# Performance work log

Hardware: AMD Instinct MI355X
Metric: run time of the kernel (lower is better)

The kernel has to match this reference:

```python
import jax, jax.numpy as jnp
import numpy as np

B, C_IN, C_INT, C_OUT, H, W = 4, 1024, 256, 1024, 64, 64
EPS = 1e-5

def conv1x1(x, w, b):
    # x: (B, Cin, H, W), w: (Cout, Cin), b: (Cout,)
    return jnp.einsum('bchw,oc->bohw', x, w) + b[None, :, None, None]

def batchnorm_eval(x, gamma, beta, mean, var):
    inv = gamma / jnp.sqrt(var + EPS)
    return x * inv[None, :, None, None] + (beta - mean * inv)[None, :, None, None]

def setup_inputs() -> dict:
    key = jax.random.key(0)
    ks = jax.random.split(key, 8)
    s_in = 1.0 / np.sqrt(C_IN)
    s_int = 1.0 / np.sqrt(C_INT)
    return {
        'x': jax.random.normal(ks[0], (B, C_IN, H, W), dtype=jnp.float32),
        'w_key': jax.random.normal(ks[1], (C_INT, C_IN), dtype=jnp.float32) * s_in,
        'b_key': jnp.zeros((C_INT,), dtype=jnp.float32),
        'gamma': jnp.ones((C_INT,), dtype=jnp.float32),
        'beta': jnp.zeros((C_INT,), dtype=jnp.float32),
        'mean': jnp.zeros((C_INT,), dtype=jnp.float32),
        'var': jnp.ones((C_INT,), dtype=jnp.float32),
        'w_value': jax.random.normal(ks[2], (C_INT, C_IN), dtype=jnp.float32) * s_in,
        'b_value': jax.random.normal(ks[3], (C_INT,), dtype=jnp.float32) * 0.1,
        'w_out': jax.random.normal(ks[4], (C_OUT, C_INT), dtype=jnp.float32) * s_int,
        'b_out': jax.random.normal(ks[5], (C_OUT,), dtype=jnp.float32) * 0.1,
    }

def reference(x, w_key, b_key, gamma, beta, mean, var, w_value, b_value, w_out, b_out):
    Bb, _, h, w = x.shape
    N = h * w
    # value: 1x1 conv, (B, C, N) -> (B, N, C)
    value = conv1x1(x, w_value, b_value).reshape(Bb, C_INT, N).transpose(0, 2, 1)
    # query/key share the same conv+BN (f_query = f_key)
    qk = batchnorm_eval(conv1x1(x, w_key, b_key), gamma, beta, mean, var).reshape(Bb, C_INT, N)
    query = qk.transpose(0, 2, 1)  # (B, N, C)
    key = qk                        # (B, C, N)
    sim = jnp.einsum('bnc,bcm->bnm', query, key) * (C_INT ** -0.5)  # (B, N, N)
    sim = jax.nn.softmax(sim, axis=-1)
    context = jnp.einsum('bnm,bmc->bnc', sim, value)  # (B, N, C)
    context = context.transpose(0, 2, 1).reshape(Bb, C_INT, h, w)
    return conv1x1(context, w_out, b_out)
```

## Files before the change

### kernel.cpp

```cpp
#include <hip/hip_runtime.h>

#define BATCH 4
#define CIN   1024
#define CI    256
#define CO    1024
#define NSP   4096

typedef __attribute__((ext_vector_type(8))) short bf16x8;
typedef __attribute__((ext_vector_type(4))) float f32x4;
typedef __attribute__((ext_vector_type(2))) unsigned uint2v;

struct __align__(8) us4 { unsigned short x, y, z, w; };

#define DEVI __device__ __forceinline__

DEVI unsigned short f2bf(float f) {
  union { float f; unsigned u; } un; un.f = f;
  unsigned u = un.u;
  u += 0x7FFFu + ((u >> 16) & 1u);
  return (unsigned short)(u >> 16);
}

DEVI unsigned cvtpk(float lo, float hi) {
  unsigned r;
  asm("v_cvt_pk_bf16_f32 %0, %1, %2" : "=v"(r) : "v"(lo), "v"(hi));
  return r;
}

DEVI void gl2lds16(const void* g, void* l) {
  __builtin_amdgcn_global_load_lds(
      (const __attribute__((address_space(1))) void*)g,
      (__attribute__((address_space(3))) void*)l, 16, 0, 0);
}

DEVI f32x4 mfma16(bf16x8 a, bf16x8 b, f32x4 c) {
  return __builtin_amdgcn_mfma_f32_16x16x32_bf16(a, b, c, 0, 0, 0);
}

__global__ __launch_bounds__(256) void k_xpose_prep(
    const float* __restrict__ x, unsigned short* __restrict__ xT,
    const float* __restrict__ w_key, const float* __restrict__ w_val,
    const float* __restrict__ w_out,
    const float* __restrict__ gamma, const float* __restrict__ beta,
    const float* __restrict__ mean,  const float* __restrict__ var,
    const float* __restrict__ b_key,
    unsigned short* __restrict__ wkv, unsigned short* __restrict__ wob,
    float* __restrict__ sq, float* __restrict__ bq)
{
  int bid = blockIdx.x;
  if (bid < 2048) {
    int idx = bid * 256 + threadIdx.x;
    float wv = (idx < 262144) ? w_key[idx] : w_val[idx - 262144];
    wkv[idx] = f2bf(wv);
    if (idx < 262144) wob[idx] = f2bf(w_out[idx]);
    if (idx < 256) {
      float inv = gamma[idx] * rsqrtf(var[idx] + 1e-5f);
      sq[idx] = 0.25f * inv;
      bq[idx] = 0.25f * (beta[idx] + (b_key[idx] - mean[idx]) * inv);
    }
    return;
  }
  __shared__ unsigned short tile[64][66];
  int id2 = bid - 2048;
  int b = id2 >> 10, k0 = ((id2 >> 6) & 15) * 64, n0 = (id2 & 63) * 64;
  int tid = threadIdx.x;
  int rr = tid >> 4, cc = tid & 15;
  const float* xb = x + ((size_t)b * CIN + k0) * NSP + n0;
#pragma unroll
  for (int p = 0; p < 4; ++p) {
    int row = p * 16 + rr;
    float4 v = *(const float4*)(xb + (size_t)row * NSP + cc * 4);
    *(unsigned*)&tile[row][cc * 4 + 0] = cvtpk(v.x, v.y);
    *(unsigned*)&tile[row][cc * 4 + 2] = cvtpk(v.z, v.w);
  }
  __syncthreads();
  unsigned short* xtb = xT + ((size_t)b * NSP + n0) * CIN + k0;
#pragma unroll
  for (int p = 0; p < 4; ++p) {
    int n = p * 16 + rr;
    int kq = cc * 4;
    us4 pk;
    pk.x = tile[kq + 0][n]; pk.y = tile[kq + 1][n];
    pk.z = tile[kq + 2][n]; pk.w = tile[kq + 3][n];
    *(us4*)(xtb + (size_t)n * CIN + kq) = pk;
  }
}

template<int KDIM>
DEVI void gemm_core_db(const unsigned short* __restrict__ Ab,
                       const unsigned short* __restrict__ Bb,
                       unsigned short* ldsA, unsigned short* ldsB,
                       f32x4 acc[4][4], int tid)
{
  const int lane = tid & 63, wave = tid >> 6;
  const int q = lane >> 4, ln = lane & 15;
  const int wm = wave & 1, wn = wave >> 1;

  int aoff[4][2], boff[4][2];
#pragma unroll
  for (int f = 0; f < 4; ++f) {
    int ra = wm * 64 + f * 16 + ln;
    aoff[f][0] = (ra * 8 + ((q)     ^ (ra & 7))) * 8;
    aoff[f][1] = (ra * 8 + ((q + 4) ^ (ra & 7))) * 8;
    int rb = wn * 64 + f * 16 + ln;
    boff[f][0] = (rb * 8 + ((q)     ^ (rb & 7))) * 8;
    boff[f][1] = (rb * 8 + ((q + 4) ^ (rb & 7))) * 8;
  }
  int sgo[4];
#pragma unroll
  for (int i = 0; i < 4; ++i) {
    int s = i * 256 + tid;
    int row = s >> 3;
    int c8 = (s & 7) ^ (row & 7);
    sgo[i] = row * KDIM + c8 * 8;
  }
#pragma unroll
  for (int i = 0; i < 4; ++i) {
    gl2lds16(Ab + sgo[i], ldsA + (i * 256 + wave * 64) * 8);
    gl2lds16(Bb + sgo[i], ldsB + (i * 256 + wave * 64) * 8);
  }
  __syncthreads();

  for (int k0 = 0; k0 < KDIM; k0 += 64) {
    const int cur = (k0 >> 6) & 1;
    unsigned short* A = ldsA + cur * (128 * 64);
    unsigned short* B = ldsB + cur * (128 * 64);
    if (k0 + 64 < KDIM) {
      unsigned short* An = ldsA + (cur ^ 1) * (128 * 64);
      unsigned short* Bn = ldsB + (cur ^ 1) * (128 * 64);
#pragma unroll
      for (int i = 0; i < 4; ++i) {
        gl2lds16(Ab + sgo[i] + k0 + 64, An + (i * 256 + wave * 64) * 8);
        gl2lds16(Bb + sgo[i] + k0 + 64, Bn + (i * 256 + wave * 64) * 8);
      }
    }
#pragma unroll
    for (int kk = 0; kk < 2; ++kk) {
      bf16x8 af[4], bfr[4];
#pragma unroll
      for (int f = 0; f < 4; ++f) af[f]  = *(const bf16x8*)(A + aoff[f][kk]);
#pragma unroll
      for (int f = 0; f < 4; ++f) bfr[f] = *(const bf16x8*)(B + boff[f][kk]);
#pragma unroll
      for (int mf = 0; mf < 4; ++mf)
#pragma unroll
        for (int nf = 0; nf < 4; ++nf)
          acc[mf][nf] = mfma16(af[mf], bfr[nf], acc[mf][nf]);
    }
    __syncthreads();
  }
}

DEVI void gemm256(const unsigned short* __restrict__ Ab,
                  const unsigned short* __restrict__ Bb,
                  unsigned short* ldsA,
                  unsigned short* ldsB,
                  f32x4 acc[8][4], int tid)
{
  const int lane = tid & 63, wave = tid >> 6;
  const int q = lane >> 4, ln = lane & 15;
  const int wm = wave & 1, wn = wave >> 1;

  int aoff[8][2], boff[4][2];
#pragma unroll
  for (int f = 0; f < 8; ++f) {
    int ra = wm * 128 + f * 16 + ln;
    aoff[f][0] = (ra * 8 + ((q)     ^ (ra & 7))) * 8;
    aoff[f][1] = (ra * 8 + ((q + 4) ^ (ra & 7))) * 8;
  }
#pragma unroll
  for (int f = 0; f < 4; ++f) {
    int rb = wn * 64 + f * 16 + ln;
    boff[f][0] = (rb * 8 + ((q)     ^ (rb & 7))) * 8;
    boff[f][1] = (rb * 8 + ((q + 4) ^ (rb & 7))) * 8;
  }
  int sgoA[8], sgoB[4];
#pragma unroll
  for (int i = 0; i < 8; ++i) {
    int s = i * 256 + tid;
    int row = s >> 3;
    int c8 = (s & 7) ^ (row & 7);
    sgoA[i] = row * CI + c8 * 8;
  }
#pragma unroll
  for (int i = 0; i < 4; ++i) {
    int s = i * 256 + tid;
    int row = s >> 3;
    int c8 = (s & 7) ^ (row & 7);
    sgoB[i] = row * CI + c8 * 8;
  }
  for (int k0 = 0; k0 < CI; k0 += 64) {
#pragma unroll
    for (int i = 0; i < 8; ++i)
      gl2lds16(Ab + sgoA[i] + k0, ldsA + (i * 256 + wave * 64) * 8);
#pragma unroll
    for (int i = 0; i < 4; ++i)
      gl2lds16(Bb + sgoB[i] + k0, ldsB + (i * 256 + wave * 64) * 8);
    __syncthreads();
#pragma unroll
    for (int kk = 0; kk < 2; ++kk) {
      bf16x8 af[8], bfr[4];
#pragma unroll
      for (int f = 0; f < 8; ++f) af[f]  = *(const bf16x8*)(ldsA + aoff[f][kk]);
#pragma unroll
      for (int f = 0; f < 4; ++f) bfr[f] = *(const bf16x8*)(ldsB + boff[f][kk]);
#pragma unroll
      for (int mf = 0; mf < 8; ++mf)
#pragma unroll
        for (int nf = 0; nf < 4; ++nf)
          acc[mf][nf] = mfma16(af[mf], bfr[nf], acc[mf][nf]);
    }
    __syncthreads();
  }
}

__global__ __launch_bounds__(256) void k_convqkv(
    const unsigned short* __restrict__ wkv,
    const unsigned short* __restrict__ xT,
    const float* __restrict__ sq, const float* __restrict__ bq,
    const float* __restrict__ bval,
    unsigned short* __restrict__ qkT,
    unsigned short* __restrict__ vv)
{
  __shared__ __align__(16) unsigned short ldsA[2 * 128 * 64];
  __shared__ __align__(16) unsigned short ldsB[2 * 128 * 64];
  int b = blockIdx.z, m0 = blockIdx.y * 128, n0 = blockIdx.x * 128;
  int tid = threadIdx.x;
  f32x4 z = {0.f, 0.f, 0.f, 0.f};
  f32x4 acc[4][4];
#pragma unroll
  for (int i = 0; i < 4; ++i)
#pragma unroll
    for (int j = 0; j < 4; ++j) acc[i][j] = z;

  const unsigned short* wp = wkv + (size_t)m0 * CIN;
  const unsigned short* xp = xT + ((size_t)b * NSP + n0) * CIN;
  bool qk = (m0 < 256);
  gemm_core_db<CIN>(qk ? wp : xp, qk ? xp : wp, ldsA, ldsB, acc, tid);

  int lane = tid & 63, wave = tid >> 6, q = lane >> 4, ln = lane & 15;
  int wm = wave & 1, wn = wave >> 1;
  if (qk) {
#pragma unroll
    for (int mf = 0; mf < 4; ++mf) {
      int cb = m0 + wm * 64 + mf * 16 + q * 4;
      float s0_ = sq[cb + 0], s1_ = sq[cb + 1], s2_ = sq[cb + 2], s3_ = sq[cb + 3];
      float b0_ = bq[cb + 0], b1_ = bq[cb + 1], b2_ = bq[cb + 2], b3_ = bq[cb + 3];
#pragma unroll
      for (int nf = 0; nf < 4; ++nf) {
        int n = n0 + wn * 64 + nf * 16 + ln;
        uint2v pk2;
        pk2.x = cvtpk(acc[mf][nf][0] * s0_ + b0_, acc[mf][nf][1] * s1_ + b1_);
        pk2.y = cvtpk(acc[mf][nf][2] * s2_ + b2_, acc[mf][nf][3] * s3_ + b3_);
        *(uint2v*)(qkT + ((size_t)b * NSP + n) * CI + cb) = pk2;
      }
    }
  } else {
    int c0 = m0 - 256;
#pragma unroll
    for (int nf = 0; nf < 4; ++nf) {
      int c = c0 + wn * 64 + nf * 16 + ln;
      float bv = bval[c];
      unsigned short* vr = vv + ((size_t)b * CI + c) * NSP + n0 + wm * 64 + q * 4;
#pragma unroll
      for (int mf = 0; mf < 4; ++mf) {
        uint2v wv2;
        wv2.x = cvtpk(acc[mf][nf][0] + bv, acc[mf][nf][1] + bv);
        wv2.y = cvtpk(acc[mf][nf][2] + bv, acc[mf][nf][3] + bv);
        *(uint2v*)(vr + mf * 16) = wv2;
      }
    }
  }
}

__global__ __launch_bounds__(256, 2) void k_attn_part(
    const unsigned short* __restrict__ qkT,
    const unsigned short* __restrict__ vv,
    unsigned* __restrict__ Opart,
    float* __restrict__ Lpart)
{
  __shared__ __align__(16) unsigned short Kt[2][32 * 256];
  __shared__ __align__(16) unsigned short Vt[2][256 * 32];
  __shared__ __align__(16) unsigned short Pl[4 * 32 * 40];

  int bid = blockIdx.x;
  int slice = bid & 15, qt = bid >> 4;
  int b = slice >> 2, js = slice & 3;
  int n0 = qt * 128;
  int tid = threadIdx.x, lane = tid & 63, wave = tid >> 6;
  int q = lane >> 4, ln = lane & 15;
  const unsigned short* qkb = qkT + (size_t)b * NSP * CI;
  const unsigned short* vb  = vv  + (size_t)b * CI * NSP;

  bf16x8 Qf0[8], Qf1[8];
  {
    const unsigned short* qr0 = qkb + (size_t)(n0 + wave * 32 + ln) * CI + q * 8;
    const unsigned short* qr1 = qr0 + 16 * CI;
#pragma unroll
    for (int t = 0; t < 8; ++t) Qf0[t] = *(const bf16x8*)(qr0 + t * 32);
#pragma unroll
    for (int t = 0; t < 8; ++t) Qf1[t] = *(const bf16x8*)(qr1 + t * 32);
  }

  int kbA = (ln * 32 + ((q ^ (ln & 7)) & 7)) * 8;
  int kbB = (ln * 32 + (((4 + q) ^ (ln & 7)) & 7)) * 8;
  int vbase = (ln * 4 + ((q ^ ((ln >> 1) & 3)) & 3)) * 8;

  unsigned short* Plw = Pl + wave * (32 * 40);
  int pw0 = ln * 40 + q * 4;
  int pw1 = ln * 40 + 16 + q * 4;
  int pw2 = (ln + 16) * 40 + q * 4;
  int pw3 = (ln + 16) * 40 + 16 + q * 4;
  int pr0 = ln * 40 + q * 8;
  int pr1 = (ln + 16) * 40 + q * 8;

  int gko[4], gvo[4];
#pragma unroll
  for (int i = 0; i < 4; ++i) {
    int s = i * 256 + tid;
    int j = s >> 5, f = s & 31;
    gko[i] = j * CI + ((f & 24) | ((f ^ j) & 7)) * 8;
    int c = s >> 2;
    gvo[i] = c * NSP + ((s ^ (c >> 1)) & 3) * 8;
  }

  f32x4 O0[16], O1[16];
  f32x4 z = {0.f, 0.f, 0.f, 0.f};
#pragma unroll
  for (int cf = 0; cf < 16; ++cf) { O0[cf] = z; O1[cf] = z; }
  float l0c = 0.f, l1c = 0.f;

  int jbase = js * 1024;

#pragma unroll
  for (int i = 0; i < 4; ++i)
    gl2lds16(qkb + (size_t)jbase * CI + gko[i], &Kt[0][(i * 256 + wave * 64) * 8]);
#pragma unroll
  for (int i = 0; i < 4; ++i)
    gl2lds16(vb + jbase + gvo[i], &Vt[0][(i * 256 + wave * 64) * 8]);
  __syncthreads();

  for (int it = 0; it < 32; ++it) {
    int cur = it & 1;

    if (it < 31) {
      int j1 = jbase + (it + 1) * 32;
#pragma unroll
      for (int i = 0; i < 4; ++i)
        gl2lds16(qkb + (size_t)j1 * CI + gko[i],
                 &Kt[cur ^ 1][(i * 256 + wave * 64) * 8]);
#pragma unroll
      for (int i = 0; i < 4; ++i)
        gl2lds16(vb + j1 + gvo[i],
                 &Vt[cur ^ 1][(i * 256 + wave * 64) * 8]);
    }

    const unsigned short* Kc = Kt[cur];
    const unsigned short* Vc = Vt[cur];

    f32x4 s0 = z, s1 = z, s2 = z, s3 = z;
    __builtin_amdgcn_s_setprio(1);
#pragma unroll
    for (int t = 0; t < 8; ++t) {
      int ko = ((t & 1) ? kbB : kbA) + (t >> 1) * 64;
      bf16x8 kf0 = *(const bf16x8*)(Kc + ko);
      bf16x8 kf1 = *(const bf16x8*)(Kc + ko + 4096);
      s0 = mfma16(kf0, Qf0[t], s0);
      s1 = mfma16(kf1, Qf0[t], s1);
      s2 = mfma16(kf0, Qf1[t], s2);
      s3 = mfma16(kf1, Qf1[t], s3);
    }
    __builtin_amdgcn_s_setprio(0);

    float p00 = __expf(s0[0]), p01 = __expf(s0[1]);
    float p02 = __expf(s0[2]), p03 = __expf(s0[3]);
    float p04 = __expf(s1[0]), p05 = __expf(s1[1]);
    float p06 = __expf(s1[2]), p07 = __expf(s1[3]);
    float p10 = __expf(s2[0]), p11 = __expf(s2[1]);
    float p12 = __expf(s2[2]), p13 = __expf(s2[3]);
    float p14 = __expf(s3[0]), p15 = __expf(s3[1]);
    float p16 = __expf(s3[2]), p17 = __expf(s3[3]);

    uint2v w;
    w.x = cvtpk(p00, p01); w.y = cvtpk(p02, p03);
    *(uint2v*)(Plw + pw0) = w;
    w.x = cvtpk(p04, p05); w.y = cvtpk(p06, p07);
    *(uint2v*)(Plw + pw1) = w;
    w.x = cvtpk(p10, p11); w.y = cvtpk(p12, p13);
    *(uint2v*)(Plw + pw2) = w;
    w.x = cvtpk(p14, p15); w.y = cvtpk(p16, p17);
    *(uint2v*)(Plw + pw3) = w;

    l0c += ((p00 + p01) + (p02 + p03)) + ((p04 + p05) + (p06 + p07));
    l1c += ((p10 + p11) + (p12 + p13)) + ((p14 + p15) + (p16 + p17));

    bf16x8 pf0 = *(const bf16x8*)(Plw + pr0);
    bf16x8 pf1 = *(const bf16x8*)(Plw + pr1);
    __builtin_amdgcn_s_setprio(1);
#pragma unroll
    for (int cf = 0; cf < 16; ++cf) {
      bf16x8 vf = *(const bf16x8*)(Vc + vbase + cf * 512);
      O0[cf] = mfma16(pf0, vf, O0[cf]);
      O1[cf] = mfma16(pf1, vf, O1[cf]);
    }
    __builtin_amdgcn_s_setprio(0);

    __syncthreads();
  }

  l0c += __shfl_xor(l0c, 16); l0c += __shfl_xor(l0c, 32);
  l1c += __shfl_xor(l1c, 16); l1c += __shfl_xor(l1c, 32);

  unsigned* Ob = Opart + (size_t)bid * (64 * 256);
  if (lane < 16) {
    Lpart[bid * 128 + wave * 32 + lane] = l0c;
    Lpart[bid * 128 + wave * 32 + 16 + lane] = l1c;
  }
#pragma unroll
  for (int r = 0; r < 4; ++r) {
    int rp = wave * 16 + q * 4 + r;
#pragma unroll
    for (int cf = 0; cf < 16; ++cf)
      Ob[rp * 256 + cf * 16 + ln] = cvtpk(O0[cf][r], O1[cf][r]);
  }
}

__global__ __launch_bounds__(256) void k_merge(
    const unsigned* __restrict__ Opart,
    const float* __restrict__ Lpart,
    unsigned short* __restrict__ ctx)
{
  __shared__ float Winv[64];
  int mb = blockIdx.x;
  int b = mb >> 6, qg = mb & 63;
  int qt = qg >> 1, half = qg & 1;
  int tid = threadIdx.x;
  int pb0 = qt * 16 + b * 4;

  if (tid < 64) {
    int row = half * 64 + tid;
    float L = Lpart[(pb0 + 0) * 128 + row]
            + Lpart[(pb0 + 1) * 128 + row]
            + Lpart[(pb0 + 2) * 128 + row]
            + Lpart[(pb0 + 3) * 128 + row];
    Winv[tid] = 1.0f / L;
  }
  __syncthreads();

  const unsigned* P0 = Opart + ((size_t)(pb0 + 0) * 64 + half * 32) * 256;
  const unsigned* P1 = Opart + ((size_t)(pb0 + 1) * 64 + half * 32) * 256;
  const unsigned* P2 = Opart + ((size_t)(pb0 + 2) * 64 + half * 32) * 256;
  const unsigned* P3 = Opart + ((size_t)(pb0 + 3) * 64 + half * 32) * 256;
  unsigned short* cb = ctx + ((size_t)b * NSP + qg * 64) * CI;
#pragma unroll 4
  for (int rp = 0; rp < 32; ++rp) {
    unsigned u0 = P0[rp * 256 + tid], u1 = P1[rp * 256 + tid];
    unsigned u2 = P2[rp * 256 + tid], u3 = P3[rp * 256 + tid];
    float lo = __uint_as_float(u0 << 16) + __uint_as_float(u1 << 16)
             + __uint_as_float(u2 << 16) + __uint_as_float(u3 << 16);
    float hi = __uint_as_float(u0 & 0xFFFF0000u) + __uint_as_float(u1 & 0xFFFF0000u)
             + __uint_as_float(u2 & 0xFFFF0000u) + __uint_as_float(u3 & 0xFFFF0000u);
    int ra = (rp & 15) + ((rp >> 4) << 5);
    int rb = ra + 16;
    cb[(size_t)ra * CI + tid] = f2bf(lo * Winv[ra]);
    cb[(size_t)rb * CI + tid] = f2bf(hi * Winv[rb]);
  }
}

__global__ __launch_bounds__(256) void k_convout(
    const unsigned short* __restrict__ wo,
    const unsigned short* __restrict__ ctx,
    const float* __restrict__ bout,
    float* __restrict__ out)
{
  __shared__ __align__(16) unsigned short ldsA[256 * 64];
  __shared__ __align__(16) unsigned short ldsB[128 * 64];
  int b = blockIdx.z, m0 = blockIdx.y * 256, n0 = blockIdx.x * 128;
  int tid = threadIdx.x;
  f32x4 z = {0.f, 0.f, 0.f, 0.f};
  f32x4 acc[8][4];
#pragma unroll
  for (int i = 0; i < 8; ++i)
#pragma unroll
    for (int j = 0; j < 4; ++j) acc[i][j] = z;

  gemm256(wo + (size_t)m0 * CI, ctx + ((size_t)b * NSP + n0) * CI,
          ldsA, ldsB, acc, tid);

  int lane = tid & 63, wave = tid >> 6, q = lane >> 4, ln = lane & 15;
  int wm = wave & 1, wn = wave >> 1;
#pragma unroll
  for (int mf = 0; mf < 8; ++mf) {
    int cb = m0 + wm * 128 + mf * 16 + q * 4;
    float bo0 = bout[cb + 0], bo1 = bout[cb + 1], bo2 = bout[cb + 2], bo3 = bout[cb + 3];
#pragma unroll
    for (int nf = 0; nf < 4; ++nf) {
      int n = n0 + wn * 64 + nf * 16 + ln;
      float* p = out + ((size_t)b * CO + cb) * NSP + n;
      p[0 * (size_t)NSP] = acc[mf][nf][0] + bo0;
      p[1 * (size_t)NSP] = acc[mf][nf][1] + bo1;
      p[2 * (size_t)NSP] = acc[mf][nf][2] + bo2;
      p[3 * (size_t)NSP] = acc[mf][nf][3] + bo3;
    }
  }
}

extern "C" void kernel_launch(void* const* d_in, const int* in_sizes, int n_in,
                              void* d_out, int out_size, void* d_ws, size_t ws_size,
                              hipStream_t stream) {
  const float* x     = (const float*)d_in[0];
  const float* w_key = (const float*)d_in[1];
  const float* b_key = (const float*)d_in[2];
  const float* gamma = (const float*)d_in[3];
  const float* beta  = (const float*)d_in[4];
  const float* mean  = (const float*)d_in[5];
  const float* var   = (const float*)d_in[6];
  const float* w_val = (const float*)d_in[7];
  const float* b_val = (const float*)d_in[8];
  const float* w_out = (const float*)d_in[9];
  const float* b_out = (const float*)d_in[10];
  float* out = (float*)d_out;

  char* ws = (char*)d_ws;
  unsigned short* xT  = (unsigned short*)(ws);
  unsigned short* wkv = (unsigned short*)(ws + 33554432);
  unsigned short* wob = (unsigned short*)(ws + 34603008);
  unsigned short* qkT = (unsigned short*)(ws + 35127296);
  unsigned short* vv  = (unsigned short*)(ws + 43515904);
  unsigned short* ctx = (unsigned short*)(ws + 51904512);
  float* sq = (float*)(ws + 60293120);
  float* bq = (float*)(ws + 60294144);
  unsigned* Opart = (unsigned*)(ws + 60295168);
  float* Lpart = (float*)(ws + 127404032);

  k_xpose_prep<<<6144, 256, 0, stream>>>(x, xT, w_key, w_val, w_out, gamma,
                                         beta, mean, var, b_key, wkv, wob,
                                         sq, bq);
  k_convqkv<<<dim3(32, 4, 4), 256, 0, stream>>>(wkv, xT, sq, bq, b_val, qkT, vv);
  k_attn_part<<<512, 256, 0, stream>>>(qkT, vv, Opart, Lpart);
  k_merge<<<256, 256, 0, stream>>>(Opart, Lpart, ctx);
  k_convout<<<dim3(32, 4, 4), 256, 0, stream>>>(wob, ctx, b_out, out);
}
```

Baseline: 258.6 us.

## Enlarge conv GEMM tiles to 512-thread blocks with double-buffered LDS

The QKV conv becomes a 256x128 tile per 512-thread block: the query/key half reuses the full 256-row key weight across a 128-pixel tile, and the value half uses a 256-pixel by 128-channel tile. The output conv moves to 256x256 tiles with 512 threads and gains double-buffered LDS prefetch of the next K slice, which it lacked before. s_setprio is raised around the MFMA sections in both kernels. The aim is more data reuse per LDS load and better overlap of memory with compute, at the cost of fewer blocks (256 each), more LDS per block and possible occupancy or register pressure.

Result: no change. 263.4 us (+1.9%).

```diff
diff --git a/kernel.cpp b/kernel.cpp
--- a/kernel.cpp
+++ b/kernel.cpp
@@ -86,15 +86,36 @@
   }
 }
 
-template<int KDIM>
-DEVI void gemm_core_db(const unsigned short* __restrict__ Ab,
-                       const unsigned short* __restrict__ Bb,
-                       unsigned short* ldsA, unsigned short* ldsB,
-                       f32x4 acc[4][4], int tid)
+__global__ __launch_bounds__(512, 2) void k_convqkv(
+    const unsigned short* __restrict__ wkv,
+    const unsigned short* __restrict__ xT,
+    const float* __restrict__ sq, const float* __restrict__ bq,
+    const float* __restrict__ bval,
+    unsigned short* __restrict__ qkT,
+    unsigned short* __restrict__ vv)
 {
+  __shared__ __align__(16) unsigned short ldsA[2 * 256 * 64];
+  __shared__ __align__(16) unsigned short ldsB[2 * 128 * 64];
+
+  int bid = blockIdx.x;
+  int tid = threadIdx.x;
   const int lane = tid & 63, wave = tid >> 6;
   const int q = lane >> 4, ln = lane & 15;
-  const int wm = wave & 1, wn = wave >> 1;
+  const int wm = wave & 3, wn = wave >> 2;
+
+  bool qk = (bid < 128);
+  const unsigned short *Ab, *Bb;
+  int b, n0, ch = 0;
+  if (qk) {
+    n0 = (bid & 31) * 128; b = bid >> 5;
+    Ab = wkv;
+    Bb = xT + ((size_t)b * NSP + n0) * CIN;
+  } else {
+    int id2 = bid - 128;
+    n0 = (id2 & 15) * 256; ch = ((id2 >> 4) & 1) * 128; b = id2 >> 5;
+    Ab = xT + ((size_t)b * NSP + n0) * CIN;
+    Bb = wkv + (size_t)(256 + ch) * CIN;
+  }
 
   int aoff[4][2], boff[4][2];
 #pragma unroll
@@ -106,34 +127,52 @@
     boff[f][0] = (rb * 8 + ((q)     ^ (rb & 7))) * 8;
     boff[f][1] = (rb * 8 + ((q + 4) ^ (rb & 7))) * 8;
   }
-  int sgo[4];
+  int sgA[4], sgB[2];
 #pragma unroll
   for (int i = 0; i < 4; ++i) {
-    int s = i * 256 + tid;
+    int s = i * 512 + tid;
     int row = s >> 3;
     int c8 = (s & 7) ^ (row & 7);
-    sgo[i] = row * KDIM + c8 * 8;
-  }
-#pragma unroll
-  for (int i = 0; i < 4; ++i) {
-    gl2lds16(Ab + sgo[i], ldsA + (i * 256 + wave * 64) * 8);
-    gl2lds16(Bb + sgo[i], ldsB + (i * 256 + wave * 64) * 8);
-  }
+    sgA[i] = row * CIN + c8 * 8;
+  }
+#pragma unroll
+  for (int i = 0; i < 2; ++i) {
+    int s = i * 512 + tid;
+    int row = s >> 3;
+    int c8 = (s & 7) ^ (row & 7);
+    sgB[i] = row * CIN + c8 * 8;
+  }
+
+#pragma unroll
+  for (int i = 0; i < 4; ++i)
+    gl2lds16(Ab + sgA[i], ldsA + (i * 512 + wave * 64) * 8);
+#pragma unroll
+  for (int i = 0; i < 2; ++i)
+    gl2lds16(Bb + sgB[i], ldsB + (i * 512 + wave * 64) * 8);
   __syncthreads();
 
-  for (int k0 = 0; k0 < KDIM; k0 += 64) {
+  f32x4 z = {0.f, 0.f, 0.f, 0.f};
+  f32x4 acc[4][4];
+#pragma unroll
+  for (int i = 0; i < 4; ++i)
+#pragma unroll
+    for (int j = 0; j < 4; ++j) acc[i][j] = z;
+
+  for (int k0 = 0; k0 < CIN; k0 += 64) {
     const int cur = (k0 >> 6) & 1;
-    unsigned short* A = ldsA + cur * (128 * 64);
-    unsigned short* B = ldsB + cur * (128 * 64);
-    if (k0 + 64 < KDIM) {
-      unsigned short* An = ldsA + (cur ^ 1) * (128 * 64);
+    const unsigned short* A = ldsA + cur * (256 * 64);
+    const unsigned short* B = ldsB + cur * (128 * 64);
+    if (k0 + 64 < CIN) {
+      unsigned short* An = ldsA + (cur ^ 1) * (256 * 64);
       unsigned short* Bn = ldsB + (cur ^ 1) * (128 * 64);
 #pragma unroll
-      for (int i = 0; i < 4; ++i) {
-        gl2lds16(Ab + sgo[i] + k0 + 64, An + (i * 256 + wave * 64) * 8);
-        gl2lds16(Bb + sgo[i] + k0 + 64, Bn + (i * 256 + wave * 64) * 8);
-      }
-    }
+      for (int i = 0; i < 4; ++i)
+        gl2lds16(Ab + sgA[i] + k0 + 64, An + (i * 512 + wave * 64) * 8);
+#pragma unroll
+      for (int i = 0; i < 2; ++i)
+        gl2lds16(Bb + sgB[i] + k0 + 64, Bn + (i * 512 + wave * 64) * 8);
+    }
+    __builtin_amdgcn_s_setprio(1);
 #pragma unroll
     for (int kk = 0; kk < 2; ++kk) {
       bf16x8 af[4], bfr[4];
@@ -147,103 +186,14 @@
         for (int nf = 0; nf < 4; ++nf)
           acc[mf][nf] = mfma16(af[mf], bfr[nf], acc[mf][nf]);
     }
+    __builtin_amdgcn_s_setprio(0);
     __syncthreads();
   }
-}
-
-DEVI void gemm256(const unsigned short* __restrict__ Ab,
-                  const unsigned short* __restrict__ Bb,
-                  unsigned short* ldsA,
-                  unsigned short* ldsB,
-                  f32x4 acc[8][4], int tid)
-{
-  const int lane = tid & 63, wave = tid >> 6;
-  const int q = lane >> 4, ln = lane & 15;
-  const int wm = wave & 1, wn = wave >> 1;
-
-  int aoff[8][2], boff[4][2];
-#pragma unroll
-  for (int f = 0; f < 8; ++f) {
-    int ra = wm * 128 + f * 16 + ln;
-    aoff[f][0] = (ra * 8 + ((q)     ^ (ra & 7))) * 8;
-    aoff[f][1] = (ra * 8 + ((q + 4) ^ (ra & 7))) * 8;
-  }
-#pragma unroll
-  for (int f = 0; f < 4; ++f) {
-    int rb = wn * 64 + f * 16 + ln;
-    boff[f][0] = (rb * 8 + ((q)     ^ (rb & 7))) * 8;
-    boff[f][1] = (rb * 8 + ((q + 4) ^ (rb & 7))) * 8;
-  }
-  int sgoA[8], sgoB[4];
-#pragma unroll
-  for (int i = 0; i < 8; ++i) {
-    int s = i * 256 + tid;
-    int row = s >> 3;
-    int c8 = (s & 7) ^ (row & 7);
-    sgoA[i] = row * CI + c8 * 8;
-  }
-#pragma unroll
-  for (int i = 0; i < 4; ++i) {
-    int s = i * 256 + tid;
-    int row = s >> 3;
-    int c8 = (s & 7) ^ (row & 7);
-    sgoB[i] = row * CI + c8 * 8;
-  }
-  for (int k0 = 0; k0 < CI; k0 += 64) {
-#pragma unroll
-    for (int i = 0; i < 8; ++i)
-      gl2lds16(Ab + sgoA[i] + k0, ldsA + (i * 256 + wave * 64) * 8);
-#pragma unroll
-    for (int i = 0; i < 4; ++i)
-      gl2lds16(Bb + sgoB[i] + k0, ldsB + (i * 256 + wave * 64) * 8);
-    __syncthreads();
-#pragma unroll
-    for (int kk = 0; kk < 2; ++kk) {
-      bf16x8 af[8], bfr[4];
-#pragma unroll
-      for (int f = 0; f < 8; ++f) af[f]  = *(const bf16x8*)(ldsA + aoff[f][kk]);
-#pragma unroll
-      for (int f = 0; f < 4; ++f) bfr[f] = *(const bf16x8*)(ldsB + boff[f][kk]);
-#pragma unroll
-      for (int mf = 0; mf < 8; ++mf)
-#pragma unroll
-        for (int nf = 0; nf < 4; ++nf)
-          acc[mf][nf] = mfma16(af[mf], bfr[nf], acc[mf][nf]);
-    }
-    __syncthreads();
-  }
-}
-
-__global__ __launch_bounds__(256) void k_convqkv(
-    const unsigned short* __restrict__ wkv,
-    const unsigned short* __restrict__ xT,
-    const float* __restrict__ sq, const float* __restrict__ bq,
-    const float* __restrict__ bval,
-    unsigned short* __restrict__ qkT,
-    unsigned short* __restrict__ vv)
-{
-  __shared__ __align__(16) unsigned short ldsA[2 * 128 * 64];
-  __shared__ __align__(16) unsigned short ldsB[2 * 128 * 64];
-  int b = blockIdx.z, m0 = blockIdx.y * 128, n0 = blockIdx.x * 128;
-  int tid = threadIdx.x;
-  f32x4 z = {0.f, 0.f, 0.f, 0.f};
-  f32x4 acc[4][4];
-#pragma unroll
-  for (int i = 0; i < 4; ++i)
-#pragma unroll
-    for (int j = 0; j < 4; ++j) acc[i][j] = z;
-
-  const unsigned short* wp = wkv + (size_t)m0 * CIN;
-  const unsigned short* xp = xT + ((size_t)b * NSP + n0) * CIN;
-  bool qk = (m0 < 256);
-  gemm_core_db<CIN>(qk ? wp : xp, qk ? xp : wp, ldsA, ldsB, acc, tid);
-
-  int lane = tid & 63, wave = tid >> 6, q = lane >> 4, ln = lane & 15;
-  int wm = wave & 1, wn = wave >> 1;
+
   if (qk) {
 #pragma unroll
     for (int mf = 0; mf < 4; ++mf) {
-      int cb = m0 + wm * 64 + mf * 16 + q * 4;
+      int cb = wm * 64 + mf * 16 + q * 4;
       float s0_ = sq[cb + 0], s1_ = sq[cb + 1], s2_ = sq[cb + 2], s3_ = sq[cb + 3];
       float b0_ = bq[cb + 0], b1_ = bq[cb + 1], b2_ = bq[cb + 2], b3_ = bq[cb + 3];
 #pragma unroll
@@ -256,10 +206,9 @@
       }
     }
   } else {
-    int c0 = m0 - 256;
 #pragma unroll
     for (int nf = 0; nf < 4; ++nf) {
-      int c = c0 + wn * 64 + nf * 16 + ln;
+      int c = ch + wn * 64 + nf * 16 + ln;
       float bv = bval[c];
       unsigned short* vr = vv + ((size_t)b * CI + c) * NSP + n0 + wm * 64 + q * 4;
 #pragma unroll
@@ -467,16 +416,52 @@
   }
 }
 
-__global__ __launch_bounds__(256) void k_convout(
+__global__ __launch_bounds__(512, 2) void k_convout(
     const unsigned short* __restrict__ wo,
     const unsigned short* __restrict__ ctx,
     const float* __restrict__ bout,
     float* __restrict__ out)
 {
-  __shared__ __align__(16) unsigned short ldsA[256 * 64];
-  __shared__ __align__(16) unsigned short ldsB[128 * 64];
-  int b = blockIdx.z, m0 = blockIdx.y * 256, n0 = blockIdx.x * 128;
+  __shared__ __align__(16) unsigned short ldsA[2 * 256 * 64];
+  __shared__ __align__(16) unsigned short ldsB[2 * 256 * 64];
+  int b = blockIdx.z, m0 = blockIdx.y * 256, n0 = blockIdx.x * 256;
   int tid = threadIdx.x;
+  const int lane = tid & 63, wave = tid >> 6;
+  const int q = lane >> 4, ln = lane & 15;
+  const int wm = wave & 1, wn = wave >> 1;
+
+  const unsigned short* Ab = wo + (size_t)m0 * CI;
+  const unsigned short* Bb = ctx + ((size_t)b * NSP + n0) * CI;
+
+  int aoff[8][2], boff[4][2];
+#pragma unroll
+  for (int f = 0; f < 8; ++f) {
+    int ra = wm * 128 + f * 16 + ln;
+    aoff[f][0] = (ra * 8 + ((q)     ^ (ra & 7))) * 8;
+    aoff[f][1] = (ra * 8 + ((q + 4) ^ (ra & 7))) * 8;
+  }
+#pragma unroll
+  for (int f = 0; f < 4; ++f) {
+    int rb = wn * 64 + f * 16 + ln;
+    boff[f][0] = (rb * 8 + ((q)     ^ (rb & 7))) * 8;
+    boff[f][1] = (rb * 8 + ((q + 4) ^ (rb & 7))) * 8;
+  }
+  int sg[4];
+#pragma unroll
+  for (int i = 0; i < 4; ++i) {
+    int s = i * 512 + tid;
+    int row = s >> 3;
+    int c8 = (s & 7) ^ (row & 7);
+    sg[i] = row * CI + c8 * 8;
+  }
+
+#pragma unroll
+  for (int i = 0; i < 4; ++i) {
+    gl2lds16(Ab + sg[i], ldsA + (i * 512 + wave * 64) * 8);
+    gl2lds16(Bb + sg[i], ldsB + (i * 512 + wave * 64) * 8);
+  }
+  __syncthreads();
+
   f32x4 z = {0.f, 0.f, 0.f, 0.f};
   f32x4 acc[8][4];
 #pragma unroll
@@ -484,11 +469,37 @@
 #pragma unroll
     for (int j = 0; j < 4; ++j) acc[i][j] = z;
 
-  gemm256(wo + (size_t)m0 * CI, ctx + ((size_t)b * NSP + n0) * CI,
-          ldsA, ldsB, acc, tid);
-
-  int lane = tid & 63, wave = tid >> 6, q = lane >> 4, ln = lane & 15;
-  int wm = wave & 1, wn = wave >> 1;
+  for (int k0 = 0; k0 < CI; k0 += 64) {
+    const int cur = (k0 >> 6) & 1;
+    const unsigned short* A = ldsA + cur * (256 * 64);
+    const unsigned short* B = ldsB + cur * (256 * 64);
+    if (k0 + 64 < CI) {
+      unsigned short* An = ldsA + (cur ^ 1) * (256 * 64);
+      unsigned short* Bn = ldsB + (cur ^ 1) * (256 * 64);
+#pragma unroll
+      for (int i = 0; i < 4; ++i) {
+        gl2lds16(Ab + sg[i] + k0 + 64, An + (i * 512 + wave * 64) * 8);
+        gl2lds16(Bb + sg[i] + k0 + 64, Bn + (i * 512 + wave * 64) * 8);
+      }
+    }
+    __builtin_amdgcn_s_setprio(1);
+#pragma unroll
+    for (int kk = 0; kk < 2; ++kk) {
+      bf16x8 af[8], bfr[4];
+#pragma unroll
+      for (int f = 0; f < 8; ++f) af[f]  = *(const bf16x8*)(A + aoff[f][kk]);
+#pragma unroll
+      for (int f = 0; f < 4; ++f) bfr[f] = *(const bf16x8*)(B + boff[f][kk]);
+#pragma unroll
+      for (int mf = 0; mf < 8; ++mf)
+#pragma unroll
+        for (int nf = 0; nf < 4; ++nf)
+          acc[mf][nf] = mfma16(af[mf], bfr[nf], acc[mf][nf]);
+    }
+    __builtin_amdgcn_s_setprio(0);
+    __syncthreads();
+  }
+
 #pragma unroll
   for (int mf = 0; mf < 8; ++mf) {
     int cb = m0 + wm * 128 + mf * 16 + q * 4;
@@ -536,8 +547,8 @@
   k_xpose_prep<<<6144, 256, 0, stream>>>(x, xT, w_key, w_val, w_out, gamma,
                                          beta, mean, var, b_key, wkv, wob,
                                          sq, bq);
-  k_convqkv<<<dim3(32, 4, 4), 256, 0, stream>>>(wkv, xT, sq, bq, b_val, qkT, vv);
+  k_convqkv<<<256, 512, 0, stream>>>(wkv, xT, sq, bq, b_val, qkT, vv);
   k_attn_part<<<512, 256, 0, stream>>>(qkT, vv, Opart, Lpart);
   k_merge<<<256, 256, 0, stream>>>(Opart, Lpart, ctx);
-  k_convout<<<dim3(32, 4, 4), 256, 0, stream>>>(wob, ctx, b_out, out);
-}
+  k_convout<<<dim3(16, 4, 4), 512, 0, stream>>>(wob, ctx, b_out, out);
+}
```
